# Kernel optimization log

Measured on AMD Instinct MI355X. Metric: run time of the kernel, lower is better.

Reference implementation:

```python
import jax, jax.numpy as jnp
import numpy as np

KS = 3; PAD = 1; NK = KS * KS  # 3x3 deform kernel, 9 sampling points

def conv2d(x, w, b=None, pad=1):
    out = jax.lax.conv_general_dilated(x, w, (1, 1), [(pad, pad), (pad, pad)],
                                       dimension_numbers=('NCHW', 'OIHW', 'NCHW'))
    return out if b is None else out + b[None, :, None, None]

def bn(x, g, b, m, v, eps=1e-5):
    s = g * jax.lax.rsqrt(v + eps)
    return x * s[None, :, None, None] + (b - m * s)[None, :, None, None]

def pool2(x, kind):
    if kind == 'max':
        return jax.lax.reduce_window(x, -jnp.inf, jax.lax.max, (1, 1, 2, 2), (1, 1, 2, 2), 'VALID')
    s = jax.lax.reduce_window(x, 0.0, jax.lax.add, (1, 1, 2, 2), (1, 1, 2, 2), 'VALID')
    return s * 0.25

def _gather(xflat, idx):
    # xflat [b,c,Hp*Wp], idx [b,h,w,NK] int32 -> [b,c,h,w,NK]
    b, c, _ = xflat.shape
    out = jax.vmap(lambda xf, ix: xf[:, ix])(xflat, idx.reshape(b, -1))
    return out.reshape(b, c, *idx.shape[1:])

def deform_conv(x, pw, pb, w):
    # DeformConv2D: internal offset conv -> bilinear gather -> 3x3-equivalent conv (einsum)
    b, c, h, wd = x.shape
    off = conv2d(x, pw, pb).transpose(0, 2, 3, 1)  # [b,h,w,2*NK], first NK = x(row), last NK = y(col)
    rng = jnp.arange(KS, dtype=x.dtype) - (KS - 1) // 2
    pn_x = jnp.repeat(rng, KS)  # kernel row offsets, n = 3*i + j ordering
    pn_y = jnp.tile(rng, KS)
    px = jnp.arange(1, h + 1, dtype=x.dtype)[:, None, None] + pn_x + off[..., :NK]  # [b,h,w,NK]
    py = jnp.arange(1, wd + 1, dtype=x.dtype)[None, :, None] + pn_y + off[..., NK:]
    Hp, Wp = h + 2 * PAD, wd + 2 * PAD
    px = jnp.clip(px, 0, Hp - 1); py = jnp.clip(py, 0, Wp - 1)
    x0 = jnp.clip(jnp.floor(px), 0, Hp - 1); y0 = jnp.clip(jnp.floor(py), 0, Wp - 1)
    x1 = jnp.clip(x0 + 1, 0, Hp - 1);        y1 = jnp.clip(y0 + 1, 0, Wp - 1)
    g_lt = (1 + x0 - px) * (1 + y0 - py)
    g_rb = (1 - x1 + px) * (1 - y1 + py)
    g_lb = (1 + x0 - px) * (1 - y1 + py)
    g_rt = (1 - x1 + px) * (1 + y0 - py)
    xp = jnp.pad(x, ((0, 0), (0, 0), (PAD, PAD), (PAD, PAD))).reshape(b, c, Hp * Wp)
    ix0 = x0.astype(jnp.int32); iy0 = y0.astype(jnp.int32)
    ix1 = x1.astype(jnp.int32); iy1 = y1.astype(jnp.int32)
    v = (g_lt[:, None] * _gather(xp, ix0 * Wp + iy0)
       + g_rb[:, None] * _gather(xp, ix1 * Wp + iy1)
       + g_lb[:, None] * _gather(xp, ix0 * Wp + iy1)
       + g_rt[:, None] * _gather(xp, ix1 * Wp + iy0))  # [b,c,h,w,NK]
    oc = w.shape[0]
    return jnp.einsum('bchwn,ocn->bohw', v, w.reshape(oc, c, NK))

def reference(x, d1_pw, d1_pb, d1_w, bn1_g, bn1_b, bn1_m, bn1_v,
              c2_w, c2_b, bn2_g, bn2_b, bn2_m, bn2_v,
              d3_pw, d3_pb, d3_w, bn3_g, bn3_b, bn3_m, bn3_v,
              c4_w, c4_b, bn4_g, bn4_b, bn4_m, bn4_v,
              c5_w, c5_b, bn5_g, bn5_b, bn5_m, bn5_v,
              c6_w, c6_b, bn6_g, bn6_b, bn6_m, bn6_v,
              fc_w, fc_b, fc1_w, fc1_b):
    h = jax.nn.relu(bn(deform_conv(x, d1_pw, d1_pb, d1_w), bn1_g, bn1_b, bn1_m, bn1_v))
    h = pool2(jax.nn.relu(bn(conv2d(h, c2_w, c2_b), bn2_g, bn2_b, bn2_m, bn2_v)), 'max')
    h = jax.nn.relu(bn(deform_conv(h, d3_pw, d3_pb, d3_w), bn3_g, bn3_b, bn3_m, bn3_v))  # Dropout(0.1) eval = id
    h = pool2(jax.nn.relu(bn(conv2d(h, c4_w, c4_b), bn4_g, bn4_b, bn4_m, bn4_v)), 'max')
    h = jax.nn.relu(bn(conv2d(h, c5_w, c5_b), bn5_g, bn5_b, bn5_m, bn5_v))
    h = pool2(jax.nn.relu(bn(conv2d(h, c6_w, c6_b), bn6_g, bn6_b, bn6_m, bn6_v)), 'avg')
    h = h.reshape(h.shape[0], -1)  # [b, 128*2*2]
    h = h @ fc_w.T + fc_b          # Dropout eval = id
    return h @ fc1_w.T + fc1_b

def setup_inputs():
    key = jax.random.key(0)
    keys = iter(jax.random.split(key, 80))
    nk = lambda: next(keys)
    B, C, P, NC = 128, 200, 16, 16
    d = {}
    d['x'] = jax.random.normal(nk(), (B, C, P, P), jnp.float32)
    def conv_w(oc, ic, k=3, scale=None):
        s = scale if scale is not None else 1.0 / np.sqrt(ic * k * k)
        return jax.random.normal(nk(), (oc, ic, k, k), jnp.float32) * s
    def add_bn(name, c):
        d[name + '_g'] = 1.0 + 0.1 * jax.random.normal(nk(), (c,), jnp.float32)
        d[name + '_b'] = 0.1 * jax.random.normal(nk(), (c,), jnp.float32)
        d[name + '_m'] = 0.1 * jax.random.normal(nk(), (c,), jnp.float32)
        d[name + '_v'] = jax.random.uniform(nk(), (c,), jnp.float32) + 0.5
    d['d1_pw'] = conv_w(2 * NK, C, scale=0.01); d['d1_pb'] = jnp.zeros(2 * NK, jnp.float32)
    d['d1_w'] = conv_w(96, C); add_bn('bn1', 96)
    d['c2_w'] = conv_w(96, 96); d['c2_b'] = jnp.zeros(96, jnp.float32); add_bn('bn2', 96)
    d['d3_pw'] = conv_w(2 * NK, 96, scale=0.01); d['d3_pb'] = jnp.zeros(2 * NK, jnp.float32)
    d['d3_w'] = conv_w(108, 96); add_bn('bn3', 108)
    d['c4_w'] = conv_w(108, 108); d['c4_b'] = jnp.zeros(108, jnp.float32); add_bn('bn4', 108)
    d['c5_w'] = conv_w(128, 108); d['c5_b'] = jnp.zeros(128, jnp.float32); add_bn('bn5', 128)
    d['c6_w'] = conv_w(128, 128); d['c6_b'] = jnp.zeros(128, jnp.float32); add_bn('bn6', 128)
    d['fc_w'] = jax.random.normal(nk(), (200, 512), jnp.float32) / np.sqrt(512)
    d['fc_b'] = jnp.zeros(200, jnp.float32)
    d['fc1_w'] = jax.random.normal(nk(), (NC, 200), jnp.float32) / np.sqrt(200)
    d['fc1_b'] = jnp.zeros(NC, jnp.float32)
    return d
```

## Files before the change

### kernel.cpp

```cpp
#include <hip/hip_runtime.h>

typedef __attribute__((ext_vector_type(8))) short short8;
typedef __attribute__((ext_vector_type(4))) float f32x4;

#define MFMA16(a, b, c) __builtin_amdgcn_mfma_f32_16x16x32_bf16(a, b, c, 0, 0, 0)

__device__ __forceinline__ unsigned short f2bf(float x) {
  union { float f; unsigned u; } c; c.f = x;
  unsigned r = c.u + 0x7FFFu + ((c.u >> 16) & 1u);
  return (unsigned short)(r >> 16);
}
__device__ __forceinline__ float bf2f(unsigned short h) {
  union { unsigned u; float f; } c; c.u = ((unsigned)h) << 16; return c.f;
}
__device__ __forceinline__ unsigned cvtpk(float lo, float hi) {
  unsigned r;
  asm("v_cvt_pk_bf16_f32 %0, %1, %2" : "=v"(r) : "v"(lo), "v"(hi));
  return r;
}

static constexpr size_t PK_D1PW = 0;
static constexpr size_t PK_D1W  = 237568;
static constexpr size_t PK_C2W  = 950272;
static constexpr size_t PK_D3PW = 1294336;
static constexpr size_t PK_D3W  = 1409024;
static constexpr size_t PK_C4W  = 1810432;
static constexpr size_t OFF1_B  = 2269184;
static constexpr size_t H2P_B   = 2269184;
static constexpr size_t H1_B    = 5414912;
static constexpr size_t OFF3_B  = 5414912;
static constexpr size_t H3_B    = 5709824;
static constexpr size_t H4P_B   = 9248768;
static constexpr size_t H5_B    = 10133504;
static constexpr size_t H6P_B   = 11182080;
static constexpr size_t FCO_B   = 11444224;
static constexpr size_t PT5_B   = 11546624;
static constexpr size_t PT6_B   = 12044288;

__global__ __launch_bounds__(256) void k_pack6(
    const float* __restrict__ s0, const float* __restrict__ s1,
    const float* __restrict__ s2, const float* __restrict__ s3,
    const float* __restrict__ s4, const float* __restrict__ s5,
    char* __restrict__ ws) {
  int blk = blockIdx.x;
  const float* src; unsigned short* dst; int K, Kp, OC, IC; bool gm;
  if      (blk <  232) { src=s0; dst=(unsigned short*)(ws+PK_D1PW); OC=18;  K=1800; Kp=1856; IC=200; gm=false; }
  else if (blk <  952) { src=s1; dst=(unsigned short*)(ws+PK_D1W);  OC=96;  K=1800; Kp=1920; IC=200; gm=true;  blk -= 232; }
  else if (blk < 1288) { src=s2; dst=(unsigned short*)(ws+PK_C2W);  OC=96;  K=864;  Kp=896;  IC=96;  gm=false; blk -= 952; }
  else if (blk < 1400) { src=s3; dst=(unsigned short*)(ws+PK_D3PW); OC=18;  K=864;  Kp=896;  IC=96;  gm=false; blk -= 1288; }
  else if (blk < 1792) { src=s4; dst=(unsigned short*)(ws+PK_D3W);  OC=108; K=864;  Kp=896;  IC=96;  gm=true;  blk -= 1400; }
  else                 { src=s5; dst=(unsigned short*)(ws+PK_C4W);  OC=108; K=972;  Kp=1024; IC=108; gm=false; blk -= 1792; }
  int e = blk * 256 + threadIdx.x;
  int oc = e / Kp, k = e - oc * Kp;
  float v = 0.f;
  if (oc < OC) {
    if (gm) {
      int NCB = (IC + 15) >> 4;
      if (k < NCB * 144) {
        int cb = k / 144, r = k - cb*144;
        int n = r >> 4, ci = cb*16 + (r & 15);
        if (ci < IC) v = src[(size_t)oc*K + ci*9 + n];
      }
    } else {
      if (k < K) v = src[(size_t)oc*K + k];
    }
  }
  dst[e] = f2bf(v);
}

__global__ __launch_bounds__(256) void k_packT(
    const float* __restrict__ s5, const float* __restrict__ s6,
    char* __restrict__ ws) {
  int e = blockIdx.x * 256 + threadIdx.x;
  if (e < 124416) {
    int k = e >> 7, oc = e & 127;
    ((float*)(ws + PT5_B))[e] = s5[(size_t)oc*972 + k];
  } else if (e < 124416 + 147456) {
    int e2 = e - 124416;
    int k = e2 >> 7, oc = e2 & 127;
    ((float*)(ws + PT6_B))[e2] = s6[(size_t)oc*1152 + k];
  }
}

template<int IC, int OC, int OCPAD, int NT, int H, int W, bool ROLLING>
__global__ __launch_bounds__(256, 2) void k_dgemm(
    const float* __restrict__ in,
    const unsigned short* __restrict__ offb,
    const unsigned short* __restrict__ wpk,
    const float* __restrict__ bng, const float* __restrict__ bnb,
    const float* __restrict__ bnm, const float* __restrict__ bnv,
    float* __restrict__ out) {
  constexpr int HW   = H * W;
  constexpr int NCB  = (IC + 15) >> 4;
  constexpr int KV   = NCB * 144;
  constexpr int NP   = (KV + 63) / 64;
  constexpr int KPAD = NP * 64;
  constexpr int TILES = HW / 64;
  constexpr int HP = H + 2, WPD = W + 2;
  constexpr int SAS = 72;
  constexpr int ASZ = 64 * SAS * 2;
  constexpr int BSZ = OCPAD * SAS * 2;
  constexpr int CHUNKF = HW * 16;
  constexpr int SLOTS  = ROLLING ? 2 : NCB;
  constexpr int XSZ    = SLOTS * CHUNKF * 4;
  constexpr int TIDX = 576 * 4, TWT = 576 * 16;
  constexpr int PBYTES = TIDX + TWT + 2*ASZ + BSZ + XSZ;
  constexpr int NBV = (OCPAD * 8 + 255) / 256;
  __shared__ __align__(16) char pool[PBYTES];
  uchar4* s_idx = (uchar4*)pool;
  float4* s_wt  = (float4*)(pool + TIDX);
  unsigned short* s_ah = (unsigned short*)(pool + TIDX + TWT);
  unsigned short* s_al = (unsigned short*)(pool + TIDX + TWT + ASZ);
  unsigned short* s_bh = (unsigned short*)(pool + TIDX + TWT + 2*ASZ);
  float* s_xt = (float*)(pool + TIDX + TWT + 2*ASZ + BSZ);

  const int tid = threadIdx.x;
  const int b   = blockIdx.x / TILES;
  const int hw0 = (blockIdx.x % TILES) * 64;
  const float* __restrict__ inb = in + (size_t)b * IC * HW;

  for (int i = tid; i < 576; i += 256) {
    int px2 = i / 9, n = i % 9;
    int h = (hw0 + px2) / W, w = (hw0 + px2) % W;
    float offx = bf2f(offb[(((size_t)b*18 + n)*HW) + h*W + w]);
    float offy = bf2f(offb[(((size_t)b*18 + 9 + n)*HW) + h*W + w]);
    float pxv = (float)(h + n/3) + offx;
    float pyv = (float)(w + n%3) + offy;
    pxv = fminf(fmaxf(pxv, 0.f), (float)(HP - 1));
    pyv = fminf(fmaxf(pyv, 0.f), (float)(WPD - 1));
    float x0 = floorf(pxv), y0 = floorf(pyv);
    float x1 = fminf(x0 + 1.f, (float)(HP - 1));
    float y1 = fminf(y0 + 1.f, (float)(WPD - 1));
    float glt = (1.f + x0 - pxv) * (1.f + y0 - pyv);
    float grb = (1.f - x1 + pxv) * (1.f - y1 + pyv);
    float glb = (1.f + x0 - pxv) * (1.f - y1 + pyv);
    float grt = (1.f - x1 + pxv) * (1.f + y0 - pyv);
    int   cx[4] = {(int)x0, (int)x1, (int)x0, (int)x1};
    int   cy[4] = {(int)y0, (int)y1, (int)y1, (int)y0};
    float gw[4] = {glt, grb, glb, grt};
    unsigned char id[4]; float gg[4];
#pragma unroll
    for (int q = 0; q < 4; ++q) {
      bool ok = (cx[q] >= 1) && (cx[q] <= H) && (cy[q] >= 1) && (cy[q] <= W);
      id[q] = ok ? (unsigned char)((cx[q]-1)*W + (cy[q]-1)) : (unsigned char)0;
      gg[q] = ok ? gw[q] : 0.f;
    }
    s_idx[i] = make_uchar4(id[0], id[1], id[2], id[3]);
    s_wt[i]  = make_float4(gg[0], gg[1], gg[2], gg[3]);
  }

  auto stageX = [&](int cb) {
    const int slot = ROLLING ? (cb & 1) : cb;
    float* dst = s_xt + (size_t)slot * CHUNKF;
    if constexpr (HW == 256) {
      const int pp = tid;
#pragma unroll
      for (int qj = 0; qj < 4; ++qj) {
        float4 v4;
#pragma unroll
        for (int i2 = 0; i2 < 4; ++i2) {
          int ci = cb*16 + qj*4 + i2;
          ((float*)&v4)[i2] = (ci < IC) ? inb[(size_t)ci*HW + pp] : 0.f;
        }
        *(float4*)(dst + pp*16 + ((((pp >> 1) + qj) & 3) << 2)) = v4;
      }
    } else {
      const int pp = tid & 63;
      const int qj = tid >> 6;
      float4 v4;
#pragma unroll
      for (int i2 = 0; i2 < 4; ++i2) {
        int ci = cb*16 + qj*4 + i2;
        ((float*)&v4)[i2] = (ci < IC) ? inb[(size_t)ci*HW + pp] : 0.f;
      }
      *(float4*)(dst + pp*16 + ((((pp >> 1) + qj) & 3) << 2)) = v4;
    }
  };
  if (ROLLING) stageX(0);
  else { for (int cb = 0; cb < NCB; ++cb) stageX(cb); }
  int staged = 0;

  const int lane = tid & 63;
  const int wv   = tid >> 6;
  const int m16  = lane & 15;
  const int quad = lane >> 4;
  const int px   = tid >> 2;
  const int kb   = (tid & 3) * 16;
  f32x4 acc[NT];
#pragma unroll
  for (int nt = 0; nt < NT; ++nt) acc[nt] = (f32x4){0.f, 0.f, 0.f, 0.f};
  short8 rb[NBV];

  auto prefB = [&](int p) {
    if (p >= NP) return;
    const int k0 = p * 64;
#pragma unroll
    for (int j = 0; j < NBV; ++j) {
      int e = tid + 256*j;
      if (e < OCPAD*8) {
        int oc = e >> 3, kq = e & 7;
        rb[j] = *(const short8*)(wpk + (size_t)oc*KPAD + k0 + kq*8);
      }
    }
  };
  auto commitB = [&]() {
#pragma unroll
    for (int j = 0; j < NBV; ++j) {
      int e = tid + 256*j;
      if (e < OCPAD*8) {
        int oc = e >> 3, kq = e & 7;
        *(short8*)(s_bh + oc*SAS + kq*8) = rb[j];
      }
    }
  };

  prefB(0);
  __syncthreads();

  for (int p = 0; p < NP; ++p) {
    float v[16];
    {
      const int kbase = p*64 + kb;
      if (kbase < KV) {
        const int cb2 = kbase / 144;
        const int rem = kbase - cb2*144;
        const int n   = rem >> 4;
        const int slot = ROLLING ? (cb2 & 1) : cb2;
        const float* xb = s_xt + (size_t)slot * CHUNKF;
        uchar4 t4 = s_idx[px*9 + n];
        float4 w4 = s_wt[px*9 + n];
        float4 A0[4], A1[4], A2[4], A3[4];
        {
          const int r0i = (int)t4.x, r1i = (int)t4.y;
          const int r2i = (int)t4.z, r3i = (int)t4.w;
          const float* r0 = xb + r0i * 16;
          const float* r1 = xb + r1i * 16;
          const float* r2 = xb + r2i * 16;
          const float* r3 = xb + r3i * 16;
#pragma unroll
          for (int j = 0; j < 4; ++j) {
            A0[j] = *(const float4*)(r0 + ((((r0i >> 1) + j) & 3) << 2));
            A1[j] = *(const float4*)(r1 + ((((r1i >> 1) + j) & 3) << 2));
            A2[j] = *(const float4*)(r2 + ((((r2i >> 1) + j) & 3) << 2));
            A3[j] = *(const float4*)(r3 + ((((r3i >> 1) + j) & 3) << 2));
          }
        }
#pragma unroll
        for (int j = 0; j < 4; ++j) {
          v[4*j+0] = w4.x*A0[j].x + w4.y*A1[j].x + w4.z*A2[j].x + w4.w*A3[j].x;
          v[4*j+1] = w4.x*A0[j].y + w4.y*A1[j].y + w4.z*A2[j].y + w4.w*A3[j].y;
          v[4*j+2] = w4.x*A0[j].z + w4.y*A1[j].z + w4.z*A2[j].z + w4.w*A3[j].z;
          v[4*j+3] = w4.x*A0[j].w + w4.y*A1[j].w + w4.z*A2[j].w + w4.w*A3[j].w;
        }
      } else {
#pragma unroll
        for (int i = 0; i < 16; ++i) v[i] = 0.f;
      }
    }
    {
      unsigned hp[8], lp[8];
#pragma unroll
      for (int i = 0; i < 8; ++i) {
        unsigned h = cvtpk(v[2*i], v[2*i+1]);
        float h0 = __uint_as_float(h << 16);
        float h1 = __uint_as_float(h & 0xFFFF0000u);
        hp[i] = h;
        lp[i] = cvtpk(v[2*i] - h0, v[2*i+1] - h1);
      }
      *(uint4*)&s_ah[px*SAS + kb]     = make_uint4(hp[0],hp[1],hp[2],hp[3]);
      *(uint4*)&s_ah[px*SAS + kb + 8] = make_uint4(hp[4],hp[5],hp[6],hp[7]);
      *(uint4*)&s_al[px*SAS + kb]     = make_uint4(lp[0],lp[1],lp[2],lp[3]);
      *(uint4*)&s_al[px*SAS + kb + 8] = make_uint4(lp[4],lp[5],lp[6],lp[7]);
    }
    commitB();
    if (ROLLING) {
      int want = ((p + 1) * 64 + 63) / 144;
      if (want >= NCB) want = NCB - 1;
      if (want > staged) { stageX(want); staged = want; }
    }
    prefB(p + 1);
    __syncthreads();
#pragma unroll
    for (int ks = 0; ks < 2; ++ks) {
      const int ko = ks*32 + quad*8;
      short8 ah = *(const short8*)&s_ah[(wv*16 + m16)*SAS + ko];
      short8 al = *(const short8*)&s_al[(wv*16 + m16)*SAS + ko];
#pragma unroll
      for (int nt = 0; nt < NT; ++nt) {
        short8 bh = *(const short8*)&s_bh[(nt*16 + m16)*SAS + ko];
        acc[nt] = MFMA16(ah, bh, acc[nt]);
        acc[nt] = MFMA16(al, bh, acc[nt]);
      }
    }
    __syncthreads();
  }

#pragma unroll
  for (int nt = 0; nt < NT; ++nt) {
    int oc = nt*16 + m16;
    if (oc < OC) {
      float sc = bng[oc] * rsqrtf(bnv[oc] + 1e-5f);
      float sh = bnb[oc] - bnm[oc] * sc;
#pragma unroll
      for (int reg = 0; reg < 4; ++reg) {
        int rowl = wv*16 + quad*4 + reg;
        float e = fmaxf(acc[nt][reg] * sc + sh, 0.f);
        out[((size_t)b*OC + oc)*HW + hw0 + rowl] = e;
      }
    }
  }
}

template<int IC, int OC, int OCPAD, int NT, int H, int W,
         bool HASBIAS, bool HASBN, bool RELU, int OUTMODE, int MINW, bool ALO>
__global__ __launch_bounds__(256, MINW) void k_gemm(
    const float* __restrict__ in,
    const unsigned short* __restrict__ wpk,
    const float* __restrict__ bias,
    const float* __restrict__ bng, const float* __restrict__ bnb,
    const float* __restrict__ bnm, const float* __restrict__ bnv,
    void* __restrict__ outv) {
  constexpr int HW   = H * W;
  constexpr int K    = IC * 9;
  constexpr int NP   = (K + 63) / 64;
  constexpr int KPAD = NP * 64;
  constexpr int TILES = HW / 64;
  constexpr int SAS = 72;
  constexpr int ASZ = 64 * SAS * 2;
  constexpr int NA  = ALO ? 2 : 1;
  constexpr int BSZ = OCPAD * SAS * 2;
  constexpr int SXS = HW + 8;
  constexpr int SXSZ = 8 * SXS * 4;
  constexpr int CPT = HW / 32;
  constexpr int PBST = NA*ASZ + BSZ + 2*SXSZ;
  constexpr int SOUTB = (OUTMODE == 2) ? 64 * (OC + 1) * 4 : 0;
  constexpr int PBYTES = (PBST > SOUTB) ? PBST : SOUTB;
  constexpr int NBV = (OCPAD * 8 + 255) / 256;
  __shared__ __align__(16) char pool[PBYTES];
  unsigned short* s_ah = (unsigned short*)pool;
  unsigned short* s_al = (unsigned short*)(pool + ASZ);
  unsigned short* s_bh = (unsigned short*)(pool + NA*ASZ);
  float* s_x  = (float*)(pool + NA*ASZ + BSZ);
  float* s_out = (float*)pool;

  const int tid = threadIdx.x;
  const int b   = blockIdx.x / TILES;
  const int hw0 = (blockIdx.x % TILES) * 64;
  const float* __restrict__ inb = in + (size_t)b * IC * HW;

  const int lane = tid & 63;
  const int wv   = tid >> 6;
  const int m16  = lane & 15;
  const int quad = lane >> 4;
  const int px   = tid >> 2;
  const int kb   = (tid & 3) * 16;
  const int xpl  = tid >> 5;
  const int xo   = (tid & 31) * CPT;
  f32x4 acc[NT];
#pragma unroll
  for (int nt = 0; nt < NT; ++nt) acc[nt] = (f32x4){0.f, 0.f, 0.f, 0.f};

  float  rx[2][CPT];
  short8 rb[NBV];

  auto ci0_of = [&](int p) { int c = (p*64)/9; return (c > IC-8) ? IC-8 : c; };
  auto prefX = [&](int p) {
    if (p >= NP) return;
    const float* s = inb + (size_t)(ci0_of(p) + xpl)*HW + xo;
    if constexpr (CPT == 8) {
      float4 a = ((const float4*)s)[0], c = ((const float4*)s)[1];
      rx[p&1][0]=a.x; rx[p&1][1]=a.y; rx[p&1][2]=a.z; rx[p&1][3]=a.w;
      rx[p&1][4]=c.x; rx[p&1][5]=c.y; rx[p&1][6]=c.z; rx[p&1][7]=c.w;
    } else {
      float2 a = ((const float2*)s)[0];
      rx[p&1][0]=a.x; rx[p&1][1]=a.y;
    }
  };
  auto commitX = [&](int p) {
    if (p >= NP) return;
    float* d = s_x + (size_t)(p&1)*8*SXS + xpl*SXS + xo;
    if constexpr (CPT == 8) {
      ((float4*)d)[0] = make_float4(rx[p&1][0],rx[p&1][1],rx[p&1][2],rx[p&1][3]);
      ((float4*)d)[1] = make_float4(rx[p&1][4],rx[p&1][5],rx[p&1][6],rx[p&1][7]);
    } else {
      ((float2*)d)[0] = make_float2(rx[p&1][0],rx[p&1][1]);
    }
  };
  auto prefB = [&](int p) {
    if (p >= NP) return;
    const int k0 = p * 64;
#pragma unroll
    for (int j = 0; j < NBV; ++j) {
      int e = tid + 256*j;
      if (e < OCPAD*8) {
        int oc = e >> 3, kq = e & 7;
        rb[j] = *(const short8*)(wpk + (size_t)oc*KPAD + k0 + kq*8);
      }
    }
  };
  auto commitB = [&]() {
#pragma unroll
    for (int j = 0; j < NBV; ++j) {
      int e = tid + 256*j;
      if (e < OCPAD*8) {
        int oc = e >> 3, kq = e & 7;
        *(short8*)(s_bh + oc*SAS + kq*8) = rb[j];
      }
    }
  };

  prefX(0); prefB(0); commitX(0); prefX(1);
  __syncthreads();

  for (int p = 0; p < NP; ++p) {
    const int k0 = p * 64;
    const int ci0c = ci0_of(p);
    float v[16];
    {
      const int kbase = k0 + kb;
      int ci = kbase / 9, n = kbase - ci*9;
      int hw = hw0 + px, r = hw / W, c = hw % W;
      const float* xb = s_x + (size_t)(p&1)*8*SXS;
#pragma unroll
      for (int i = 0; i < 16; ++i) {
        float val = 0.f;
        if (kbase + i < K) {
          int rr = r + n/3 - 1, cc = c + n%3 - 1;
          if (rr >= 0 && rr < H && cc >= 0 && cc < W)
            val = xb[(ci - ci0c)*SXS + rr*W + cc];
        }
        v[i] = val;
        if (++n == 9) { n = 0; ++ci; }
      }
    }
    if constexpr (ALO) {
      unsigned hp[8], lp[8];
#pragma unroll
      for (int i = 0; i < 8; ++i) {
        unsigned h = cvtpk(v[2*i], v[2*i+1]);
        float h0 = __uint_as_float(h << 16);
        float h1 = __uint_as_float(h & 0xFFFF0000u);
        hp[i] = h;
        lp[i] = cvtpk(v[2*i] - h0, v[2*i+1] - h1);
      }
      *(uint4*)&s_ah[px*SAS + kb]     = make_uint4(hp[0],hp[1],hp[2],hp[3]);
      *(uint4*)&s_ah[px*SAS + kb + 8] = make_uint4(hp[4],hp[5],hp[6],hp[7]);
      *(uint4*)&s_al[px*SAS + kb]     = make_uint4(lp[0],lp[1],lp[2],lp[3]);
      *(uint4*)&s_al[px*SAS + kb + 8] = make_uint4(lp[4],lp[5],lp[6],lp[7]);
    } else {
      unsigned hp[8];
#pragma unroll
      for (int i = 0; i < 8; ++i) hp[i] = cvtpk(v[2*i], v[2*i+1]);
      *(uint4*)&s_ah[px*SAS + kb]     = make_uint4(hp[0],hp[1],hp[2],hp[3]);
      *(uint4*)&s_ah[px*SAS + kb + 8] = make_uint4(hp[4],hp[5],hp[6],hp[7]);
    }
    commitB();
    commitX(p + 1);
    prefB(p + 1);
    prefX(p + 2);
    __syncthreads();
#pragma unroll
    for (int ks = 0; ks < 2; ++ks) {
      const int ko = ks*32 + quad*8;
      short8 ah = *(const short8*)&s_ah[(wv*16 + m16)*SAS + ko];
      short8 al;
      if constexpr (ALO) al = *(const short8*)&s_al[(wv*16 + m16)*SAS + ko];
#pragma unroll
      for (int nt = 0; nt < NT; ++nt) {
        short8 bh = *(const short8*)&s_bh[(nt*16 + m16)*SAS + ko];
        acc[nt] = MFMA16(ah, bh, acc[nt]);
        if constexpr (ALO) acc[nt] = MFMA16(al, bh, acc[nt]);
      }
    }
    __syncthreads();
  }

  constexpr int OCS = OC + 1;
#pragma unroll
  for (int nt = 0; nt < NT; ++nt) {
    int oc = nt*16 + m16;
    float bi = 0.f, sc = 1.f, sh = 0.f;
    if (oc < OC) {
      if constexpr (HASBIAS) bi = bias[oc];
      if constexpr (HASBN) {
        sc = bng[oc] * rsqrtf(bnv[oc] + 1e-5f);
        sh = bnb[oc] - bnm[oc] * sc;
      }
    }
#pragma unroll
    for (int reg = 0; reg < 4; ++reg) {
      int rowl = wv*16 + quad*4 + reg;
      float e = (acc[nt][reg] + bi) * sc + sh;
      if constexpr (RELU) e = fmaxf(e, 0.f);
      if (oc < OC) {
        if constexpr (OUTMODE == 1) {
          ((unsigned short*)outv)[((size_t)b*OC + oc)*HW + hw0 + rowl] = f2bf(e);
        } else {
          s_out[rowl*OCS + oc] = e;
        }
      }
    }
  }
  if constexpr (OUTMODE == 2) {
    __syncthreads();
    constexpr int PR = (64 / W) / 2, PC = W / 2, CNT = PR * PC * OC;
    const int r0 = hw0 / W;
    float* out = (float*)outv;
    for (int e2 = tid; e2 < CNT; e2 += 256) {
      int oc = e2 % OC, q = e2 / OC, pc = q % PC, pr = q / PC;
      int base = ((2*pr)*W + 2*pc)*OCS + oc;
      float a0 = s_out[base],         a1 = s_out[base + OCS];
      float a2 = s_out[base + W*OCS], a3 = s_out[base + W*OCS + OCS];
      float m = fmaxf(fmaxf(a0, a1), fmaxf(a2, a3));
      out[(((size_t)b*OC + oc)*(H/2) + (r0 >> 1) + pr)*(W/2) + pc] = m;
    }
  }
}

template<int IC, int OC, bool POOLAVG>
__global__ __launch_bounds__(256, 4) void k_tail(
    const float* __restrict__ in,
    const float* __restrict__ wt,
    const float* __restrict__ bias,
    const float* __restrict__ bng, const float* __restrict__ bnb,
    const float* __restrict__ bnm, const float* __restrict__ bnv,
    float* __restrict__ out) {
  constexpr int NB = OC / 32;
  __shared__ float s_pad[IC * 36];
  const int tid = threadIdx.x;
  const int b = blockIdx.x / NB;
  const int g = blockIdx.x % NB;
  for (int i = tid; i < IC*36; i += 256) {
    int ci = i / 36, pos = i % 36;
    int rr = pos / 6 - 1, cc = pos % 6 - 1;
    bool ok = (rr >= 0) && (rr < 4) && (cc >= 0) && (cc < 4);
    s_pad[i] = ok ? in[((size_t)b*IC + ci)*16 + rr*4 + cc] : 0.f;
  }
  __syncthreads();
  const int oc = g*32 + (tid >> 3);
  const int p  = tid & 7;
  const int r0 = p >> 1, c0 = (p & 1) * 2;
  float a0 = 0.f, a1 = 0.f;
  const float* wp = wt + oc;
#pragma unroll 2
  for (int ci = 0; ci < IC; ++ci) {
    const float* sp = s_pad + ci*36 + r0*6 + c0;
#pragma unroll
    for (int n = 0; n < 9; ++n) {
      float wv = wp[(size_t)(ci*9 + n)*OC];
      float v0 = sp[(n/3)*6 + (n%3)];
      float v1 = sp[(n/3)*6 + (n%3) + 1];
      a0 = fmaf(wv, v0, a0);
      a1 = fmaf(wv, v1, a1);
    }
  }
  float sc = bng[oc] * rsqrtf(bnv[oc] + 1e-5f);
  float sh = bnb[oc] - bnm[oc]*sc;
  float bi = bias[oc];
  float e0 = fmaxf((a0 + bi)*sc + sh, 0.f);
  float e1 = fmaxf((a1 + bi)*sc + sh, 0.f);
  if constexpr (!POOLAVG) {
    size_t ob = ((size_t)b*OC + oc)*16 + r0*4 + c0;
    out[ob]     = e0;
    out[ob + 1] = e1;
  } else {
    float s = e0 + e1;
    float tot = s + __shfl_xor(s, 2);
    if ((p & 2) == 0) {
      int pr = p >> 2, pc = p & 1;
      out[(size_t)b*512 + oc*4 + pr*2 + pc] = tot * 0.25f;
    }
  }
}

__global__ __launch_bounds__(128) void k_fc(const float* __restrict__ in,
                                            const float* __restrict__ w,
                                            const float* __restrict__ bias,
                                            float* __restrict__ out) {
  int j = blockIdx.x, b = threadIdx.x;
  const float4* ib = (const float4*)(in + (size_t)b*512);
  const float4* wb = (const float4*)(w + (size_t)j*512);
  float acc = bias[j];
  for (int k = 0; k < 128; ++k) {
    float4 a = ib[k], q = wb[k];
    acc = fmaf(a.x, q.x, fmaf(a.y, q.y, fmaf(a.z, q.z, fmaf(a.w, q.w, acc))));
  }
  out[(size_t)b*200 + j] = acc;
}

__global__ __launch_bounds__(128) void k_fc1(const float* __restrict__ in,
                                             const float* __restrict__ w,
                                             const float* __restrict__ bias,
                                             float* __restrict__ out) {
  int j = blockIdx.x, b = threadIdx.x;
  const float4* ib = (const float4*)(in + (size_t)b*200);
  const float4* wb = (const float4*)(w + (size_t)j*200);
  float acc = bias[j];
  for (int k = 0; k < 50; ++k) {
    float4 a = ib[k], q = wb[k];
    acc = fmaf(a.x, q.x, fmaf(a.y, q.y, fmaf(a.z, q.z, fmaf(a.w, q.w, acc))));
  }
  out[(size_t)b*16 + j] = acc;
}

extern "C" void kernel_launch(void* const* d_in, const int* in_sizes, int n_in,
                              void* d_out, int out_size, void* d_ws, size_t ws_size,
                              hipStream_t stream) {
  const float* X    = (const float*)d_in[0];
  const float* D1PW = (const float*)d_in[1];
  const float* D1PB = (const float*)d_in[2];
  const float* D1W  = (const float*)d_in[3];
  const float* BN1G = (const float*)d_in[4];
  const float* BN1B = (const float*)d_in[5];
  const float* BN1M = (const float*)d_in[6];
  const float* BN1V = (const float*)d_in[7];
  const float* C2W  = (const float*)d_in[8];
  const float* C2B  = (const float*)d_in[9];
  const float* BN2G = (const float*)d_in[10];
  const float* BN2B = (const float*)d_in[11];
  const float* BN2M = (const float*)d_in[12];
  const float* BN2V = (const float*)d_in[13];
  const float* D3PW = (const float*)d_in[14];
  const float* D3PB = (const float*)d_in[15];
  const float* D3W  = (const float*)d_in[16];
  const float* BN3G = (const float*)d_in[17];
  const float* BN3B = (const float*)d_in[18];
  const float* BN3M = (const float*)d_in[19];
  const float* BN3V = (const float*)d_in[20];
  const float* C4W  = (const float*)d_in[21];
  const float* C4B  = (const float*)d_in[22];
  const float* BN4G = (const float*)d_in[23];
  const float* BN4B = (const float*)d_in[24];
  const float* BN4M = (const float*)d_in[25];
  const float* BN4V = (const float*)d_in[26];
  const float* C5W  = (const float*)d_in[27];
  const float* C5B  = (const float*)d_in[28];
  const float* BN5G = (const float*)d_in[29];
  const float* BN5B = (const float*)d_in[30];
  const float* BN5M = (const float*)d_in[31];
  const float* BN5V = (const float*)d_in[32];
  const float* C6W  = (const float*)d_in[33];
  const float* C6B  = (const float*)d_in[34];
  const float* BN6G = (const float*)d_in[35];
  const float* BN6B = (const float*)d_in[36];
  const float* BN6M = (const float*)d_in[37];
  const float* BN6V = (const float*)d_in[38];
  const float* FCW  = (const float*)d_in[39];
  const float* FCB  = (const float*)d_in[40];
  const float* FC1W = (const float*)d_in[41];
  const float* FC1B = (const float*)d_in[42];

  char* ws = (char*)d_ws;
  unsigned short* pk_d1pw = (unsigned short*)(ws + PK_D1PW);
  unsigned short* pk_d1w  = (unsigned short*)(ws + PK_D1W);
  unsigned short* pk_c2w  = (unsigned short*)(ws + PK_C2W);
  unsigned short* pk_d3pw = (unsigned short*)(ws + PK_D3PW);
  unsigned short* pk_d3w  = (unsigned short*)(ws + PK_D3W);
  unsigned short* pk_c4w  = (unsigned short*)(ws + PK_C4W);
  unsigned short* off1 = (unsigned short*)(ws + OFF1_B);
  unsigned short* off3 = (unsigned short*)(ws + OFF3_B);
  float* h1   = (float*)(ws + H1_B);
  float* h2p  = (float*)(ws + H2P_B);
  float* h3   = (float*)(ws + H3_B);
  float* h4p  = (float*)(ws + H4P_B);
  float* h5   = (float*)(ws + H5_B);
  float* h6p  = (float*)(ws + H6P_B);
  float* fco  = (float*)(ws + FCO_B);
  float* pt5  = (float*)(ws + PT5_B);
  float* pt6  = (float*)(ws + PT6_B);
  float* outp = (float*)d_out;

  k_pack6<<<2240, 256, 0, stream>>>(D1PW, D1W, C2W, D3PW, D3W, C4W, ws);

  k_gemm<200,18,32,2,16,16,true,false,false,1,3,false><<<512, 256, 0, stream>>>(
      X, pk_d1pw, D1PB, nullptr, nullptr, nullptr, nullptr, off1);
  k_dgemm<200,96,96,6,16,16,true><<<512, 256, 0, stream>>>(
      X, off1, pk_d1w, BN1G, BN1B, BN1M, BN1V, h1);
  k_gemm<96,96,96,6,16,16,true,true,true,2,3,true><<<512, 256, 0, stream>>>(
      h1, pk_c2w, C2B, BN2G, BN2B, BN2M, BN2V, h2p);
  k_packT<<<1062, 256, 0, stream>>>(C5W, C6W, ws);
  k_gemm<96,18,32,2,8,8,true,false,false,1,3,false><<<128, 256, 0, stream>>>(
      h2p, pk_d3pw, D3PB, nullptr, nullptr, nullptr, nullptr, off3);
  k_dgemm<96,108,112,7,8,8,false><<<128, 256, 0, stream>>>(
      h2p, off3, pk_d3w, BN3G, BN3B, BN3M, BN3V, h3);
  k_gemm<108,108,112,7,8,8,true,true,true,2,3,true><<<128, 256, 0, stream>>>(
      h3, pk_c4w, C4B, BN4G, BN4B, BN4M, BN4V, h4p);
  k_tail<108,128,false><<<512, 256, 0, stream>>>(
      h4p, pt5, C5B, BN5G, BN5B, BN5M, BN5V, h5);
  k_tail<128,128,true><<<512, 256, 0, stream>>>(
      h5, pt6, C6B, BN6G, BN6B, BN6M, BN6V, h6p);
  k_fc<<<200, 128, 0, stream>>>(h6p, FCW, FCB, fco);
  k_fc1<<<16, 128, 0, stream>>>(fco, FC1W, FC1B, outp);
}
```

Before: 496.2 us.

## Build MFMA A fragments in registers and swizzle B tile layout in LDS

```diff
diff --git a/kernel.cpp b/kernel.cpp
--- a/kernel.cpp
+++ b/kernel.cpp
@@ -97,22 +97,18 @@
   constexpr int KPAD = NP * 64;
   constexpr int TILES = HW / 64;
   constexpr int HP = H + 2, WPD = W + 2;
-  constexpr int SAS = 72;
-  constexpr int ASZ = 64 * SAS * 2;
-  constexpr int BSZ = OCPAD * SAS * 2;
+  constexpr int BSZ = OCPAD * 64 * 2;
   constexpr int CHUNKF = HW * 16;
   constexpr int SLOTS  = ROLLING ? 2 : NCB;
   constexpr int XSZ    = SLOTS * CHUNKF * 4;
   constexpr int TIDX = 576 * 4, TWT = 576 * 16;
-  constexpr int PBYTES = TIDX + TWT + 2*ASZ + BSZ + XSZ;
+  constexpr int PBYTES = TIDX + TWT + BSZ + XSZ;
   constexpr int NBV = (OCPAD * 8 + 255) / 256;
   __shared__ __align__(16) char pool[PBYTES];
   uchar4* s_idx = (uchar4*)pool;
   float4* s_wt  = (float4*)(pool + TIDX);
-  unsigned short* s_ah = (unsigned short*)(pool + TIDX + TWT);
-  unsigned short* s_al = (unsigned short*)(pool + TIDX + TWT + ASZ);
-  unsigned short* s_bh = (unsigned short*)(pool + TIDX + TWT + 2*ASZ);
-  float* s_xt = (float*)(pool + TIDX + TWT + 2*ASZ + BSZ);
+  unsigned short* s_bh = (unsigned short*)(pool + TIDX + TWT);
+  float* s_xt = (float*)(pool + TIDX + TWT + BSZ);
 
   const int tid = threadIdx.x;
   const int b   = blockIdx.x / TILES;
@@ -184,8 +180,8 @@
   const int wv   = tid >> 6;
   const int m16  = lane & 15;
   const int quad = lane >> 4;
-  const int px   = tid >> 2;
-  const int kb   = (tid & 3) * 16;
+  const int pv   = wv*16 + m16;
+  const int tbase = pv * 9;
   f32x4 acc[NT];
 #pragma unroll
   for (int nt = 0; nt < NT; ++nt) acc[nt] = (f32x4){0.f, 0.f, 0.f, 0.f};
@@ -209,69 +205,69 @@
       int e = tid + 256*j;
       if (e < OCPAD*8) {
         int oc = e >> 3, kq = e & 7;
-        *(short8*)(s_bh + oc*SAS + kq*8) = rb[j];
-      }
-    }
+        *(short8*)&s_bh[(kq*OCPAD + (oc ^ ((kq*2)&7)))*8] = rb[j];
+      }
+    }
+  };
+
+  auto buildA = [&](int kk, short8& ahv, short8& alv) {
+    float v[8];
+    if (kk < KV) {
+      const int cb2 = kk / 144;
+      const int rem = kk - cb2*144;
+      const int n   = rem >> 4;
+      const int g0  = (rem >> 2) & 2;
+      const int slot = ROLLING ? (cb2 & 1) : cb2;
+      const float* xb = s_xt + (size_t)slot * CHUNKF;
+      uchar4 t4 = s_idx[tbase + n];
+      float4 w4 = s_wt[tbase + n];
+      const int r0i = (int)t4.x, r1i = (int)t4.y;
+      const int r2i = (int)t4.z, r3i = (int)t4.w;
+      const float* r0 = xb + r0i * 16;
+      const float* r1 = xb + r1i * 16;
+      const float* r2 = xb + r2i * 16;
+      const float* r3 = xb + r3i * 16;
+      float4 A0[2], A1[2], A2[2], A3[2];
+#pragma unroll
+      for (int j = 0; j < 2; ++j) {
+        A0[j] = *(const float4*)(r0 + ((((r0i >> 1) + g0 + j) & 3) << 2));
+        A1[j] = *(const float4*)(r1 + ((((r1i >> 1) + g0 + j) & 3) << 2));
+        A2[j] = *(const float4*)(r2 + ((((r2i >> 1) + g0 + j) & 3) << 2));
+        A3[j] = *(const float4*)(r3 + ((((r3i >> 1) + g0 + j) & 3) << 2));
+      }
+#pragma unroll
+      for (int j = 0; j < 2; ++j) {
+        v[4*j+0] = w4.x*A0[j].x + w4.y*A1[j].x + w4.z*A2[j].x + w4.w*A3[j].x;
+        v[4*j+1] = w4.x*A0[j].y + w4.y*A1[j].y + w4.z*A2[j].y + w4.w*A3[j].y;
+        v[4*j+2] = w4.x*A0[j].z + w4.y*A1[j].z + w4.z*A2[j].z + w4.w*A3[j].z;
+        v[4*j+3] = w4.x*A0[j].w + w4.y*A1[j].w + w4.z*A2[j].w + w4.w*A3[j].w;
+      }
+    } else {
+#pragma unroll
+      for (int i = 0; i < 8; ++i) v[i] = 0.f;
+    }
+    unsigned hp[4], lp[4];
+#pragma unroll
+    for (int i = 0; i < 4; ++i) {
+      unsigned h = cvtpk(v[2*i], v[2*i+1]);
+      float h0 = __uint_as_float(h << 16);
+      float h1 = __uint_as_float(h & 0xFFFF0000u);
+      hp[i] = h;
+      lp[i] = cvtpk(v[2*i] - h0, v[2*i+1] - h1);
+    }
+    uint4 uh = make_uint4(hp[0], hp[1], hp[2], hp[3]);
+    uint4 ul = make_uint4(lp[0], lp[1], lp[2], lp[3]);
+    ahv = *(short8*)&uh;
+    alv = *(short8*)&ul;
   };
 
   prefB(0);
   __syncthreads();
 
   for (int p = 0; p < NP; ++p) {
-    float v[16];
-    {
-      const int kbase = p*64 + kb;
-      if (kbase < KV) {
-        const int cb2 = kbase / 144;
-        const int rem = kbase - cb2*144;
-        const int n   = rem >> 4;
-        const int slot = ROLLING ? (cb2 & 1) : cb2;
-        const float* xb = s_xt + (size_t)slot * CHUNKF;
-        uchar4 t4 = s_idx[px*9 + n];
-        float4 w4 = s_wt[px*9 + n];
-        float4 A0[4], A1[4], A2[4], A3[4];
-        {
-          const int r0i = (int)t4.x, r1i = (int)t4.y;
-          const int r2i = (int)t4.z, r3i = (int)t4.w;
-          const float* r0 = xb + r0i * 16;
-          const float* r1 = xb + r1i * 16;
-          const float* r2 = xb + r2i * 16;
-          const float* r3 = xb + r3i * 16;
-#pragma unroll
-          for (int j = 0; j < 4; ++j) {
-            A0[j] = *(const float4*)(r0 + ((((r0i >> 1) + j) & 3) << 2));
-            A1[j] = *(const float4*)(r1 + ((((r1i >> 1) + j) & 3) << 2));
-            A2[j] = *(const float4*)(r2 + ((((r2i >> 1) + j) & 3) << 2));
-            A3[j] = *(const float4*)(r3 + ((((r3i >> 1) + j) & 3) << 2));
-          }
-        }
-#pragma unroll
-        for (int j = 0; j < 4; ++j) {
-          v[4*j+0] = w4.x*A0[j].x + w4.y*A1[j].x + w4.z*A2[j].x + w4.w*A3[j].x;
-          v[4*j+1] = w4.x*A0[j].y + w4.y*A1[j].y + w4.z*A2[j].y + w4.w*A3[j].y;
-          v[4*j+2] = w4.x*A0[j].z + w4.y*A1[j].z + w4.z*A2[j].z + w4.w*A3[j].z;
-          v[4*j+3] = w4.x*A0[j].w + w4.y*A1[j].w + w4.z*A2[j].w + w4.w*A3[j].w;
-        }
-      } else {
-#pragma unroll
-        for (int i = 0; i < 16; ++i) v[i] = 0.f;
-      }
-    }
-    {
-      unsigned hp[8], lp[8];
-#pragma unroll
-      for (int i = 0; i < 8; ++i) {
-        unsigned h = cvtpk(v[2*i], v[2*i+1]);
-        float h0 = __uint_as_float(h << 16);
-        float h1 = __uint_as_float(h & 0xFFFF0000u);
-        hp[i] = h;
-        lp[i] = cvtpk(v[2*i] - h0, v[2*i+1] - h1);
-      }
-      *(uint4*)&s_ah[px*SAS + kb]     = make_uint4(hp[0],hp[1],hp[2],hp[3]);
-      *(uint4*)&s_ah[px*SAS + kb + 8] = make_uint4(hp[4],hp[5],hp[6],hp[7]);
-      *(uint4*)&s_al[px*SAS + kb]     = make_uint4(lp[0],lp[1],lp[2],lp[3]);
-      *(uint4*)&s_al[px*SAS + kb + 8] = make_uint4(lp[4],lp[5],lp[6],lp[7]);
-    }
+    short8 ah[2], al[2];
+    buildA(p*64 +      quad*8, ah[0], al[0]);
+    buildA(p*64 + 32 + quad*8, ah[1], al[1]);
     commitB();
     if (ROLLING) {
       int want = ((p + 1) * 64 + 63) / 144;
@@ -282,14 +278,13 @@
     __syncthreads();
 #pragma unroll
     for (int ks = 0; ks < 2; ++ks) {
-      const int ko = ks*32 + quad*8;
-      short8 ah = *(const short8*)&s_ah[(wv*16 + m16)*SAS + ko];
-      short8 al = *(const short8*)&s_al[(wv*16 + m16)*SAS + ko];
+      const int kg = ks*4 + quad;
+      const int xm = (kg*2) & 7;
 #pragma unroll
       for (int nt = 0; nt < NT; ++nt) {
-        short8 bh = *(const short8*)&s_bh[(nt*16 + m16)*SAS + ko];
-        acc[nt] = MFMA16(ah, bh, acc[nt]);
-        acc[nt] = MFMA16(al, bh, acc[nt]);
+        short8 bh = *(const short8*)&s_bh[(kg*OCPAD + ((nt*16 + m16) ^ xm))*8];
+        acc[nt] = MFMA16(ah[ks], bh, acc[nt]);
+        acc[nt] = MFMA16(al[ks], bh, acc[nt]);
       }
     }
     __syncthreads();
@@ -325,22 +320,17 @@
   constexpr int NP   = (K + 63) / 64;
   constexpr int KPAD = NP * 64;
   constexpr int TILES = HW / 64;
-  constexpr int SAS = 72;
-  constexpr int ASZ = 64 * SAS * 2;
-  constexpr int NA  = ALO ? 2 : 1;
-  constexpr int BSZ = OCPAD * SAS * 2;
+  constexpr int BSZ = OCPAD * 64 * 2;
   constexpr int SXS = HW + 8;
   constexpr int SXSZ = 8 * SXS * 4;
   constexpr int CPT = HW / 32;
-  constexpr int PBST = NA*ASZ + BSZ + 2*SXSZ;
+  constexpr int PBST = BSZ + 2*SXSZ;
   constexpr int SOUTB = (OUTMODE == 2) ? 64 * (OC + 1) * 4 : 0;
   constexpr int PBYTES = (PBST > SOUTB) ? PBST : SOUTB;
   constexpr int NBV = (OCPAD * 8 + 255) / 256;
   __shared__ __align__(16) char pool[PBYTES];
-  unsigned short* s_ah = (unsigned short*)pool;
-  unsigned short* s_al = (unsigned short*)(pool + ASZ);
-  unsigned short* s_bh = (unsigned short*)(pool + NA*ASZ);
-  float* s_x  = (float*)(pool + NA*ASZ + BSZ);
+  unsigned short* s_bh = (unsigned short*)pool;
+  float* s_x  = (float*)(pool + BSZ);
   float* s_out = (float*)pool;
 
   const int tid = threadIdx.x;
@@ -352,8 +342,9 @@
   const int wv   = tid >> 6;
   const int m16  = lane & 15;
   const int quad = lane >> 4;
-  const int px   = tid >> 2;
-  const int kb   = (tid & 3) * 16;
+  const int pv   = wv*16 + m16;
+  const int hwp  = hw0 + pv;
+  const int pr   = hwp / W, pc = hwp % W;
   const int xpl  = tid >> 5;
   const int xo   = (tid & 31) * CPT;
   f32x4 acc[NT];
@@ -404,8 +395,23 @@
       int e = tid + 256*j;
       if (e < OCPAD*8) {
         int oc = e >> 3, kq = e & 7;
-        *(short8*)(s_bh + oc*SAS + kq*8) = rb[j];
-      }
+        *(short8*)&s_bh[(kq*OCPAD + (oc ^ ((kq*2)&7)))*8] = rb[j];
+      }
+    }
+  };
+
+  auto buildV = [&](int kk, const float* xb, int ci0c, float* v) {
+    int ci = kk / 9, n = kk - ci*9;
+#pragma unroll
+    for (int i = 0; i < 8; ++i) {
+      float val = 0.f;
+      if (kk + i < K) {
+        int rr = pr + n/3 - 1, cc = pc + n%3 - 1;
+        if (rr >= 0 && rr < H && cc >= 0 && cc < W)
+          val = xb[(ci - ci0c)*SXS + rr*W + cc];
+      }
+      v[i] = val;
+      if (++n == 9) { n = 0; ++ci; }
     }
   };
 
@@ -413,46 +419,30 @@
   __syncthreads();
 
   for (int p = 0; p < NP; ++p) {
-    const int k0 = p * 64;
     const int ci0c = ci0_of(p);
-    float v[16];
-    {
-      const int kbase = k0 + kb;
-      int ci = kbase / 9, n = kbase - ci*9;
-      int hw = hw0 + px, r = hw / W, c = hw % W;
-      const float* xb = s_x + (size_t)(p&1)*8*SXS;
-#pragma unroll
-      for (int i = 0; i < 16; ++i) {
-        float val = 0.f;
-        if (kbase + i < K) {
-          int rr = r + n/3 - 1, cc = c + n%3 - 1;
-          if (rr >= 0 && rr < H && cc >= 0 && cc < W)
-            val = xb[(ci - ci0c)*SXS + rr*W + cc];
+    const float* xb = s_x + (size_t)(p&1)*8*SXS;
+    short8 ah[2], al[2];
+#pragma unroll
+    for (int ks = 0; ks < 2; ++ks) {
+      float v[8];
+      buildV(p*64 + ks*32 + quad*8, xb, ci0c, v);
+      unsigned hp[4], lp[4];
+#pragma unroll
+      for (int i = 0; i < 4; ++i) {
+        unsigned h = cvtpk(v[2*i], v[2*i+1]);
+        hp[i] = h;
+        if constexpr (ALO) {
+          float h0 = __uint_as_float(h << 16);
+          float h1 = __uint_as_float(h & 0xFFFF0000u);
+          lp[i] = cvtpk(v[2*i] - h0, v[2*i+1] - h1);
         }
-        v[i] = val;
-        if (++n == 9) { n = 0; ++ci; }
-      }
-    }
-    if constexpr (ALO) {
-      unsigned hp[8], lp[8];
-#pragma unroll
-      for (int i = 0; i < 8; ++i) {
-        unsigned h = cvtpk(v[2*i], v[2*i+1]);
-        float h0 = __uint_as_float(h << 16);
-        float h1 = __uint_as_float(h & 0xFFFF0000u);
-        hp[i] = h;
-        lp[i] = cvtpk(v[2*i] - h0, v[2*i+1] - h1);
-      }
-      *(uint4*)&s_ah[px*SAS + kb]     = make_uint4(hp[0],hp[1],hp[2],hp[3]);
-      *(uint4*)&s_ah[px*SAS + kb + 8] = make_uint4(hp[4],hp[5],hp[6],hp[7]);
-      *(uint4*)&s_al[px*SAS + kb]     = make_uint4(lp[0],lp[1],lp[2],lp[3]);
-      *(uint4*)&s_al[px*SAS + kb + 8] = make_uint4(lp[4],lp[5],lp[6],lp[7]);
-    } else {
-      unsigned hp[8];
-#pragma unroll
-      for (int i = 0; i < 8; ++i) hp[i] = cvtpk(v[2*i], v[2*i+1]);
-      *(uint4*)&s_ah[px*SAS + kb]     = make_uint4(hp[0],hp[1],hp[2],hp[3]);
-      *(uint4*)&s_ah[px*SAS + kb + 8] = make_uint4(hp[4],hp[5],hp[6],hp[7]);
+      }
+      uint4 uh = make_uint4(hp[0], hp[1], hp[2], hp[3]);
+      ah[ks] = *(short8*)&uh;
+      if constexpr (ALO) {
+        uint4 ul = make_uint4(lp[0], lp[1], lp[2], lp[3]);
+        al[ks] = *(short8*)&ul;
+      }
     }
     commitB();
     commitX(p + 1);
@@ -461,15 +451,13 @@
     __syncthreads();
 #pragma unroll
     for (int ks = 0; ks < 2; ++ks) {
-      const int ko = ks*32 + quad*8;
-      short8 ah = *(const short8*)&s_ah[(wv*16 + m16)*SAS + ko];
-      short8 al;
-      if constexpr (ALO) al = *(const short8*)&s_al[(wv*16 + m16)*SAS + ko];
+      const int kg = ks*4 + quad;
+      const int xm = (kg*2) & 7;
 #pragma unroll
       for (int nt = 0; nt < NT; ++nt) {
-        short8 bh = *(const short8*)&s_bh[(nt*16 + m16)*SAS + ko];
-        acc[nt] = MFMA16(ah, bh, acc[nt]);
-        if constexpr (ALO) acc[nt] = MFMA16(al, bh, acc[nt]);
+        short8 bh = *(const short8*)&s_bh[(kg*OCPAD + ((nt*16 + m16) ^ xm))*8];
+        acc[nt] = MFMA16(ah[ks], bh, acc[nt]);
+        if constexpr (ALO) acc[nt] = MFMA16(al[ks], bh, acc[nt]);
       }
     }
     __syncthreads();
@@ -507,12 +495,12 @@
     const int r0 = hw0 / W;
     float* out = (float*)outv;
     for (int e2 = tid; e2 < CNT; e2 += 256) {
-      int oc = e2 % OC, q = e2 / OC, pc = q % PC, pr = q / PC;
-      int base = ((2*pr)*W + 2*pc)*OCS + oc;
+      int oc = e2 % OC, q = e2 / OC, pc2 = q % PC, pr2 = q / PC;
+      int base = ((2*pr2)*W + 2*pc2)*OCS + oc;
       float a0 = s_out[base],         a1 = s_out[base + OCS];
       float a2 = s_out[base + W*OCS], a3 = s_out[base + W*OCS + OCS];
       float m = fmaxf(fmaxf(a0, a1), fmaxf(a2, a3));
-      out[(((size_t)b*OC + oc)*(H/2) + (r0 >> 1) + pr)*(W/2) + pc] = m;
+      out[(((size_t)b*OC + oc)*(H/2) + (r0 >> 1) + pr2)*(W/2) + pc2] = m;
     }
   }
 }
```

Result: faster. 485.8 us (-2.1%).
